# Optimization experiments

Hardware: AMD Instinct MI355X
Metric: run time of the kernel (lower is better)

## Reference

```python
import jax, jax.numpy as jnp
import numpy as np

N_E = 16384
E_DIM = 64
GROUPS = 4
N_E_GROUP = N_E // GROUPS  # 4096
B, H, W = 16, 32, 32


def _l2norm(x):
    # matches F.normalize(p=2, dim=-1) with eps=1e-12
    n = jnp.linalg.norm(x, axis=-1, keepdims=True)
    return x / jnp.maximum(n, 1e-12)


def setup_inputs() -> dict:
    key = jax.random.key(0)
    k1, k2 = jax.random.split(key)
    z_groups = jax.random.normal(k1, (B, GROUPS * E_DIM, H, W), dtype=jnp.float32)
    emb = jax.random.uniform(k2, (N_E, E_DIM), minval=-1.0 / N_E, maxval=1.0 / N_E,
                             dtype=jnp.float32)
    emb = _l2norm(emb)  # module normalizes codebook at init when l2_norm=True
    return {"z_groups": z_groups, "embedding": emb}


def reference(z_groups, embedding):
    # Eval-mode forward (no EMA/random-restart buffer updates, losses are 0).
    b, c, h, w = z_groups.shape
    # split channels into groups: b (g*c) h w -> b h w g c
    z = z_groups.reshape(b, GROUPS, E_DIM, h, w).transpose(0, 3, 4, 1, 2)
    z = _l2norm(z)                                     # l2_norm=True path
    zf = z.reshape(-1, GROUPS, E_DIM)                  # [N, g, c]
    emb = _l2norm(embedding.reshape(GROUPS, N_E_GROUP, E_DIM))  # [g, k, c]

    # d = -|z|^2 - |e|^2 + 2 z.e  (negative squared distance), argmax = nearest
    d = (2.0 * jnp.einsum('ngc,gkc->ngk', zf, emb)
         - jnp.sum(zf * zf, axis=-1)[..., None]
         - jnp.sum(emb * emb, axis=-1)[None, :, :])    # [N, g, k]
    idx = jnp.argmax(d, axis=-1)                       # [N, g]

    zq = emb[jnp.arange(GROUPS)[None, :], idx]         # [N, g, c] gather
    zq = zf + jax.lax.stop_gradient(zq - zf)           # straight-through

    # b h w g c -> b (g*c) h w
    quant = zq.reshape(b, h, w, GROUPS, E_DIM).transpose(0, 3, 4, 1, 2)
    quant = quant.reshape(b, GROUPS * E_DIM, h, w)

    vq_loss = jnp.zeros((GROUPS,), jnp.float32)
    commit_loss = jnp.zeros((GROUPS,), jnp.float32)
    codebook_usage = jnp.zeros((GROUPS,), jnp.float32)

    # perplexity / min_encodings correspond to the last group (loop semantics)
    min_encodings = jax.nn.one_hot(idx[:, -1], N_E_GROUP, dtype=quant.dtype)
    avg_probs = jnp.mean(min_encodings, axis=0)
    perplexity = jnp.exp(-jnp.sum(avg_probs * jnp.log(avg_probs + 1e-10)))

    return (quant, vq_loss, commit_loss, codebook_usage,
            perplexity, min_encodings, idx)
```

## Files before the change

### kernel.cpp

```cpp
#include <hip/hip_runtime.h>
#include <hip/hip_bf16.h>
#include <math.h>

#define N_E      16384
#define E_DIM    64
#define GROUPS   4
#define N_E_G    4096
#define NQ       16384

#define OFF_QUANT   0L
#define OFF_VQLOSS  4194304L
#define OFF_PERP    4194316L
#define OFF_MINENC  4194317L
#define OFF_IDX     71303181L

#define WS_EN     0L
#define WS_EN2    1048576L
#define WS_ENHI   1064960L
#define WS_ZNR    1589248L
#define WS_ZHI    5783552L
#define WS_HIST   7880704L
#define WS_IDX3   7884800L

typedef float  float4v  __attribute__((ext_vector_type(4)));
typedef short  short8   __attribute__((ext_vector_type(8)));

static __device__ __forceinline__ ushort f2bf(float x) {
    __hip_bfloat16 h = __float2bfloat16(x);
    union { __hip_bfloat16 h; ushort u; } cv; cv.h = h;
    return cv.u;
}

__global__ void norm_emb_kernel(const float* __restrict__ emb,
                                float* __restrict__ en, float* __restrict__ en2,
                                ushort* __restrict__ ehi) {
    int gid  = blockIdx.x * blockDim.x + threadIdx.x;
    int code = gid >> 6;
    int lane = threadIdx.x & 63;
    if (code >= N_E) return;
    float x = emb[code * 64 + lane];
    float ss = x * x;
    #pragma unroll
    for (int off = 32; off; off >>= 1) ss += __shfl_xor(ss, off, 64);
    float v = x / fmaxf(sqrtf(ss), 1e-12f);
    en[code * 64 + lane]  = v;
    ehi[code * 64 + lane] = f2bf(v);
    float s2 = v * v;
    #pragma unroll
    for (int off = 32; off; off >>= 1) s2 += __shfl_xor(s2, off, 64);
    if (lane == 0) en2[code] = s2;
}

__global__ void norm_z_kernel(const float* __restrict__ z,
                              float* __restrict__ znr, ushort* __restrict__ zhi) {
    __shared__ float rden[256];
    const int g  = blockIdx.y;
    const int n0 = blockIdx.x * 256;
    const int t  = threadIdx.x;

    {
        int n = n0 + t, b = n >> 10, hw = n & 1023;
        const float* src = z + (size_t)b * 262144 + (size_t)g * 65536 + hw;
        float ss = 0.f;
        for (int d = 0; d < 64; ++d) {
            float x = src[(size_t)d * 1024];
            ss = fmaf(x, x, ss);
        }
        rden[t] = fmaxf(sqrtf(ss), 1e-12f);
    }
    __syncthreads();

    for (int i = t; i < 256 * 16; i += 256) {
        int ql = i >> 4, d4 = (i & 15) * 4;
        int n = n0 + ql, b = n >> 10, hw = n & 1023;
        const float* src = z + (size_t)b * 262144 + (size_t)g * 65536 + hw;
        float den = rden[ql];
        float v0 = src[(size_t)(d4 + 0) * 1024] / den;
        float v1 = src[(size_t)(d4 + 1) * 1024] / den;
        float v2 = src[(size_t)(d4 + 2) * 1024] / den;
        float v3 = src[(size_t)(d4 + 3) * 1024] / den;
        float4v f = {v0, v1, v2, v3};
        *(float4v*)(znr + ((size_t)g * NQ + n) * 64 + d4) = f;
        ushort u0 = f2bf(v0), u1 = f2bf(v1), u2 = f2bf(v2), u3 = f2bf(v3);
        ushort4 u = {u0, u1, u2, u3};
        *(ushort4*)(zhi + ((size_t)g * NQ + n) * 64 + d4) = u;
    }
}

#define CAP  64
#define TAU  0.017f
__global__ __launch_bounds__(256, 2)
void vq_cand_kernel(const ushort* __restrict__ zhi, const ushort* __restrict__ ehi,
                    const float* __restrict__ znr, const float* __restrict__ en,
                    const float* __restrict__ en2,
                    float* __restrict__ out, int* __restrict__ idx3,
                    int* __restrict__ hist) {
    __shared__ ushort eA[128 * 64];
    __shared__ int    cnt[128];
    __shared__ int    cand[128 * CAP];
    __shared__ int    bks[128];

    const int g  = blockIdx.y;
    const int q0 = blockIdx.x * 128;
    const int t  = threadIdx.x;
    const int wave = t >> 6, lane = t & 63;
    const int l15 = lane & 15, quad = lane >> 4;
    const int qhalf = wave & 1, chalf = wave >> 1;

    if (t < 128) cnt[t] = 0;

    short8 bfrag[4][2];
    {
        const ushort* zq = zhi + ((size_t)g * NQ + q0 + qhalf * 64 + l15) * 64 + quad * 8;
        #pragma unroll
        for (int u = 0; u < 4; ++u)
            #pragma unroll
            for (int ks = 0; ks < 2; ++ks)
                bfrag[u][ks] = *(const short8*)(zq + (size_t)u * 16 * 64 + ks * 32);
    }

    float Mrun[4];
    #pragma unroll
    for (int u = 0; u < 4; ++u) Mrun[u] = -3.4e38f;

    for (int tile = 0; tile < 32; ++tile) {
        const int j0 = tile * 128;
        __syncthreads();
        {
            int c = t >> 1, half = t & 1;
            const ushort* src = ehi + ((size_t)g * N_E_G + j0 + c) * 64 + half * 32;
            #pragma unroll
            for (int qq = 0; qq < 4; ++qq) {
                int chunk = half * 4 + qq;
                short8 v = *(const short8*)(src + qq * 8);
                *(short8*)&eA[c * 64 + ((chunk ^ (c & 7)) * 8)] = v;
            }
        }
        __syncthreads();

        short8 afrag[4][2];
        #pragma unroll
        for (int cs = 0; cs < 4; ++cs) {
            int c = chalf * 64 + cs * 16 + l15;
            #pragma unroll
            for (int ks = 0; ks < 2; ++ks) {
                int chunk = ks * 4 + quad;
                afrag[cs][ks] = *(const short8*)&eA[c * 64 + ((chunk ^ (c & 7)) * 8)];
            }
        }

        float4v acc[4][4];
        #pragma unroll
        for (int cs = 0; cs < 4; ++cs)
            #pragma unroll
            for (int u = 0; u < 4; ++u) {
                float4v zz = {0.f, 0.f, 0.f, 0.f};
                acc[cs][u] = __builtin_amdgcn_mfma_f32_16x16x32_bf16(
                                 afrag[cs][0], bfrag[u][0], zz, 0, 0, 0);
                acc[cs][u] = __builtin_amdgcn_mfma_f32_16x16x32_bf16(
                                 afrag[cs][1], bfrag[u][1], acc[cs][u], 0, 0, 0);
            }

        #pragma unroll
        for (int u = 0; u < 4; ++u) {
            float m = acc[0][u][0];
            #pragma unroll
            for (int cs = 0; cs < 4; ++cs)
                #pragma unroll
                for (int r = 0; r < 4; ++r) m = fmaxf(m, acc[cs][u][r]);
            float m2 = fmaxf(m, __shfl_xor(m, 16, 64));
            float m4 = fmaxf(m2, __shfl_xor(m2, 32, 64));
            Mrun[u] = fmaxf(Mrun[u], m4);
            float thr = Mrun[u] - TAU;
            if (m >= thr) {
                int ql = qhalf * 64 + u * 16 + l15;
                #pragma unroll
                for (int cs = 0; cs < 4; ++cs)
                    #pragma unroll
                    for (int r = 0; r < 4; ++r)
                        if (acc[cs][u][r] >= thr) {
                            int cidx = j0 + chalf * 64 + cs * 16 + quad * 4 + r;
                            int slot = atomicAdd(&cnt[ql], 1);
                            if (slot < CAP) cand[ql * CAP + slot] = cidx;
                        }
            }
        }
    }
    __syncthreads();

    if (t < 128) {
        int q = q0 + t;
        float za[64];
        const float4v* zp = (const float4v*)(znr + ((size_t)g * NQ + q) * 64);
        #pragma unroll
        for (int i = 0; i < 16; ++i) {
            float4v v = zp[i];
            za[i*4+0] = v[0]; za[i*4+1] = v[1]; za[i*4+2] = v[2]; za[i*4+3] = v[3];
        }
        int nc = cnt[t]; if (nc > CAP) nc = CAP;
        float best = -3.4e38f; int bk = 0x7fffffff;
        for (int s = 0; s < nc; ++s) {
            int c = cand[t * CAP + s];
            const float* ev = en + ((size_t)g * N_E_G + c) * 64;
            float a = 0.f;
            #pragma unroll
            for (int k = 0; k < 64; ++k) a = fmaf(za[k], ev[k], a);
            float d = 2.f * a - en2[g * N_E_G + c];
            if (d > best || (d == best && c < bk)) { best = d; bk = c; }
        }
        if (bk == 0x7fffffff) bk = 0;
        bks[t] = bk;
        out[OFF_IDX + (size_t)q * 4 + g] = (float)bk;
        if (g == 3) { idx3[q] = bk; atomicAdd(&hist[bk], 1); }
    }
    __syncthreads();

    for (int i = t; i < 128 * 64; i += 256) {
        int d = i >> 7, m = i & 127;
        int n = q0 + m, b = n >> 10, hw = n & 1023;
        out[OFF_QUANT + (size_t)b * 262144 + (size_t)(g * 64 + d) * 1024 + hw] =
            en[((size_t)g * N_E_G + bks[m]) * 64 + d];
    }
}

__global__ void fill_zero_kernel(float* __restrict__ out) {
    const long n  = OFF_IDX - OFF_VQLOSS;
    const long n4 = n >> 2;
    float4v* p4 = (float4v*)(out + OFF_VQLOSS);
    long i = (long)blockIdx.x * blockDim.x + threadIdx.x;
    long stride = (long)gridDim.x * blockDim.x;
    float4v z = {0.f, 0.f, 0.f, 0.f};
    for (long j = i; j < n4; j += stride) p4[j] = z;
    if (i == 0) {
        float* p = out + OFF_VQLOSS;
        for (long j = n4 * 4; j < n; ++j) p[j] = 0.f;
    }
}

__global__ void scatter_ones_kernel(const int* __restrict__ idx3,
                                    float* __restrict__ out) {
    int r = blockIdx.x * blockDim.x + threadIdx.x;
    if (r < NQ) out[OFF_MINENC + (size_t)r * N_E_G + idx3[r]] = 1.0f;
}

__global__ void perplexity_kernel(const int* __restrict__ hist,
                                  float* __restrict__ out) {
    __shared__ float s[256];
    int t = threadIdx.x;
    float acc = 0.f;
    for (int k = t; k < N_E_G; k += 256) {
        float p = (float)hist[k] * (1.0f / 16384.0f);
        acc += p * logf(p + 1e-10f);
    }
    s[t] = acc;
    __syncthreads();
    for (int o = 128; o; o >>= 1) {
        if (t < o) s[t] += s[t + o];
        __syncthreads();
    }
    if (t == 0) out[OFF_PERP] = expf(-s[0]);
}

extern "C" void kernel_launch(void* const* d_in, const int* in_sizes, int n_in,
                              void* d_out, int out_size, void* d_ws, size_t ws_size,
                              hipStream_t stream) {
    const float* z_groups = (const float*)d_in[0];
    const float* emb      = (const float*)d_in[1];
    float* out = (float*)d_out;
    float* ws  = (float*)d_ws;

    float*  en   = ws + WS_EN;
    float*  en2  = ws + WS_EN2;
    ushort* ehi  = (ushort*)(ws + WS_ENHI);
    float*  znr  = ws + WS_ZNR;
    ushort* zhi  = (ushort*)(ws + WS_ZHI);
    int*    hist = (int*)(ws + WS_HIST);
    int*    idx3 = (int*)(ws + WS_IDX3);

    fill_zero_kernel<<<4096, 256, 0, stream>>>(out);
    norm_emb_kernel<<<N_E / 4, 256, 0, stream>>>(emb, en, en2, ehi);
    norm_z_kernel<<<dim3(NQ / 256, GROUPS), 256, 0, stream>>>(z_groups, znr, zhi);
    hipMemsetAsync(hist, 0, N_E_G * sizeof(int), stream);

    vq_cand_kernel<<<dim3(NQ / 128, GROUPS), 256, 0, stream>>>(
        zhi, ehi, znr, en, en2, out, idx3, hist);

    scatter_ones_kernel<<<NQ / 256, 256, 0, stream>>>(idx3, out);
    perplexity_kernel<<<1, 256, 0, stream>>>(hist, out);
}
```

Before: 481.0 us.

## Load codebook fragments from global with register double-buffering, fuse scatter, use memset

The candidate kernel stops staging codebook tiles through LDS with two barriers per tile. Each wave now loads its bf16 MFMA fragments straight from global memory, prefetching the next tile into a second register set. The one-hot scatter is folded into the candidate kernel, the zero-fill kernel becomes hipMemsetAsync, and z normalization goes through a padded LDS transpose so reads and writes are coalesced. The costs are higher register pressure and more global/L2 traffic for codebook reads, since waves no longer share a staged tile.

```diff
diff --git a/kernel.cpp b/kernel.cpp
--- a/kernel.cpp
+++ b/kernel.cpp
@@ -20,14 +20,12 @@
 #define WS_ZNR    1589248L
 #define WS_ZHI    5783552L
 #define WS_HIST   7880704L
-#define WS_IDX3   7884800L
 
 typedef float  float4v  __attribute__((ext_vector_type(4)));
 typedef short  short8   __attribute__((ext_vector_type(8)));
 
 static __device__ __forceinline__ ushort f2bf(float x) {
-    __hip_bfloat16 h = __float2bfloat16(x);
-    union { __hip_bfloat16 h; ushort u; } cv; cv.h = h;
+    union { __hip_bfloat16 h; ushort u; } cv; cv.h = __float2bfloat16(x);
     return cv.u;
 }
 
@@ -53,37 +51,37 @@
 
 __global__ void norm_z_kernel(const float* __restrict__ z,
                               float* __restrict__ znr, ushort* __restrict__ zhi) {
-    __shared__ float rden[256];
+    __shared__ float tile[64 * 65];
+    __shared__ float rden[64];
+
     const int g  = blockIdx.y;
-    const int n0 = blockIdx.x * 256;
+    const int n0 = blockIdx.x * 64;
     const int t  = threadIdx.x;
-
-    {
-        int n = n0 + t, b = n >> 10, hw = n & 1023;
-        const float* src = z + (size_t)b * 262144 + (size_t)g * 65536 + hw;
+    const int b  = n0 >> 10, hw0 = n0 & 1023;
+    const float* src = z + (size_t)b * 262144 + (size_t)g * 65536 + hw0;
+
+    for (int i = t; i < 4096; i += 256) {
+        int d = i >> 6, nl = i & 63;
+        tile[d * 65 + nl] = src[(size_t)d * 1024 + nl];
+    }
+    __syncthreads();
+
+    if (t < 64) {
         float ss = 0.f;
         for (int d = 0; d < 64; ++d) {
-            float x = src[(size_t)d * 1024];
+            float x = tile[d * 65 + t];
             ss = fmaf(x, x, ss);
         }
         rden[t] = fmaxf(sqrtf(ss), 1e-12f);
     }
     __syncthreads();
 
-    for (int i = t; i < 256 * 16; i += 256) {
-        int ql = i >> 4, d4 = (i & 15) * 4;
-        int n = n0 + ql, b = n >> 10, hw = n & 1023;
-        const float* src = z + (size_t)b * 262144 + (size_t)g * 65536 + hw;
-        float den = rden[ql];
-        float v0 = src[(size_t)(d4 + 0) * 1024] / den;
-        float v1 = src[(size_t)(d4 + 1) * 1024] / den;
-        float v2 = src[(size_t)(d4 + 2) * 1024] / den;
-        float v3 = src[(size_t)(d4 + 3) * 1024] / den;
-        float4v f = {v0, v1, v2, v3};
-        *(float4v*)(znr + ((size_t)g * NQ + n) * 64 + d4) = f;
-        ushort u0 = f2bf(v0), u1 = f2bf(v1), u2 = f2bf(v2), u3 = f2bf(v3);
-        ushort4 u = {u0, u1, u2, u3};
-        *(ushort4*)(zhi + ((size_t)g * NQ + n) * 64 + d4) = u;
+    for (int i = t; i < 4096; i += 256) {
+        int q = i >> 6, d = i & 63;
+        float v = tile[d * 65 + q] / rden[q];
+        size_t o = ((size_t)g * NQ + n0 + q) * 64 + d;
+        znr[o] = v;
+        zhi[o] = f2bf(v);
     }
 }
 
@@ -92,13 +90,11 @@
 __global__ __launch_bounds__(256, 2)
 void vq_cand_kernel(const ushort* __restrict__ zhi, const ushort* __restrict__ ehi,
                     const float* __restrict__ znr, const float* __restrict__ en,
-                    const float* __restrict__ en2,
-                    float* __restrict__ out, int* __restrict__ idx3,
+                    const float* __restrict__ en2, float* __restrict__ out,
                     int* __restrict__ hist) {
-    __shared__ ushort eA[128 * 64];
-    __shared__ int    cnt[128];
-    __shared__ int    cand[128 * CAP];
-    __shared__ int    bks[128];
+    __shared__ int cnt[128];
+    __shared__ int cand[128 * CAP];
+    __shared__ int bks[128];
 
     const int g  = blockIdx.y;
     const int q0 = blockIdx.x * 128;
@@ -116,51 +112,45 @@
         for (int u = 0; u < 4; ++u)
             #pragma unroll
             for (int ks = 0; ks < 2; ++ks)
-                bfrag[u][ks] = *(const short8*)(zq + (size_t)u * 16 * 64 + ks * 32);
-    }
+                bfrag[u][ks] = *(const short8*)(zq + u * 16 * 64 + ks * 32);
+    }
+    __syncthreads();
+
+    const ushort* abase = ehi + (size_t)g * N_E_G * 64
+                        + (size_t)(chalf * 64 + l15) * 64 + quad * 8;
 
     float Mrun[4];
     #pragma unroll
     for (int u = 0; u < 4; ++u) Mrun[u] = -3.4e38f;
 
-    for (int tile = 0; tile < 32; ++tile) {
-        const int j0 = tile * 128;
-        __syncthreads();
-        {
-            int c = t >> 1, half = t & 1;
-            const ushort* src = ehi + ((size_t)g * N_E_G + j0 + c) * 64 + half * 32;
-            #pragma unroll
-            for (int qq = 0; qq < 4; ++qq) {
-                int chunk = half * 4 + qq;
-                short8 v = *(const short8*)(src + qq * 8);
-                *(short8*)&eA[c * 64 + ((chunk ^ (c & 7)) * 8)] = v;
-            }
-        }
-        __syncthreads();
-
-        short8 afrag[4][2];
-        #pragma unroll
-        for (int cs = 0; cs < 4; ++cs) {
-            int c = chalf * 64 + cs * 16 + l15;
-            #pragma unroll
-            for (int ks = 0; ks < 2; ++ks) {
-                int chunk = ks * 4 + quad;
-                afrag[cs][ks] = *(const short8*)&eA[c * 64 + ((chunk ^ (c & 7)) * 8)];
-            }
-        }
-
+    short8 afA[4][2], afB[4][2];
+    #pragma unroll
+    for (int cs = 0; cs < 4; ++cs)
+        #pragma unroll
+        for (int ks = 0; ks < 2; ++ks)
+            afA[cs][ks] = *(const short8*)(abase + (size_t)(cs * 16) * 64 + ks * 32);
+
+    auto do_tile = [&](short8 (&A)[4][2], short8 (&P)[4][2], int tile) {
+        if (tile + 1 < 32) {
+            const ushort* p = abase + (size_t)((tile + 1) * 128) * 64;
+            #pragma unroll
+            for (int cs = 0; cs < 4; ++cs)
+                #pragma unroll
+                for (int ks = 0; ks < 2; ++ks)
+                    P[cs][ks] = *(const short8*)(p + (size_t)(cs * 16) * 64 + ks * 32);
+        }
         float4v acc[4][4];
         #pragma unroll
         for (int cs = 0; cs < 4; ++cs)
             #pragma unroll
             for (int u = 0; u < 4; ++u) {
                 float4v zz = {0.f, 0.f, 0.f, 0.f};
+                float4v tmp = __builtin_amdgcn_mfma_f32_16x16x32_bf16(
+                                  A[cs][0], bfrag[u][0], zz, 0, 0, 0);
                 acc[cs][u] = __builtin_amdgcn_mfma_f32_16x16x32_bf16(
-                                 afrag[cs][0], bfrag[u][0], zz, 0, 0, 0);
-                acc[cs][u] = __builtin_amdgcn_mfma_f32_16x16x32_bf16(
-                                 afrag[cs][1], bfrag[u][1], acc[cs][u], 0, 0, 0);
+                                  A[cs][1], bfrag[u][1], tmp, 0, 0, 0);
             }
-
+        const int j0 = tile * 128;
         #pragma unroll
         for (int u = 0; u < 4; ++u) {
             float m = acc[0][u][0];
@@ -185,6 +175,11 @@
                         }
             }
         }
+    };
+
+    for (int tt = 0; tt < 32; tt += 2) {
+        do_tile(afA, afB, tt);
+        do_tile(afB, afA, tt + 1);
     }
     __syncthreads();
 
@@ -211,7 +206,10 @@
         if (bk == 0x7fffffff) bk = 0;
         bks[t] = bk;
         out[OFF_IDX + (size_t)q * 4 + g] = (float)bk;
-        if (g == 3) { idx3[q] = bk; atomicAdd(&hist[bk], 1); }
+        if (g == 3) {
+            atomicAdd(&hist[bk], 1);
+            out[OFF_MINENC + (size_t)q * N_E_G + bk] = 1.0f;
+        }
     }
     __syncthreads();
 
@@ -221,26 +219,6 @@
         out[OFF_QUANT + (size_t)b * 262144 + (size_t)(g * 64 + d) * 1024 + hw] =
             en[((size_t)g * N_E_G + bks[m]) * 64 + d];
     }
-}
-
-__global__ void fill_zero_kernel(float* __restrict__ out) {
-    const long n  = OFF_IDX - OFF_VQLOSS;
-    const long n4 = n >> 2;
-    float4v* p4 = (float4v*)(out + OFF_VQLOSS);
-    long i = (long)blockIdx.x * blockDim.x + threadIdx.x;
-    long stride = (long)gridDim.x * blockDim.x;
-    float4v z = {0.f, 0.f, 0.f, 0.f};
-    for (long j = i; j < n4; j += stride) p4[j] = z;
-    if (i == 0) {
-        float* p = out + OFF_VQLOSS;
-        for (long j = n4 * 4; j < n; ++j) p[j] = 0.f;
-    }
-}
-
-__global__ void scatter_ones_kernel(const int* __restrict__ idx3,
-                                    float* __restrict__ out) {
-    int r = blockIdx.x * blockDim.x + threadIdx.x;
-    if (r < NQ) out[OFF_MINENC + (size_t)r * N_E_G + idx3[r]] = 1.0f;
 }
 
 __global__ void perplexity_kernel(const int* __restrict__ hist,
@@ -275,16 +253,15 @@
     float*  znr  = ws + WS_ZNR;
     ushort* zhi  = (ushort*)(ws + WS_ZHI);
     int*    hist = (int*)(ws + WS_HIST);
-    int*    idx3 = (int*)(ws + WS_IDX3);
-
-    fill_zero_kernel<<<4096, 256, 0, stream>>>(out);
+
+    hipMemsetAsync(out + OFF_VQLOSS, 0, (OFF_IDX - OFF_VQLOSS) * sizeof(float), stream);
+    hipMemsetAsync(hist, 0, N_E_G * sizeof(int), stream);
+
     norm_emb_kernel<<<N_E / 4, 256, 0, stream>>>(emb, en, en2, ehi);
-    norm_z_kernel<<<dim3(NQ / 256, GROUPS), 256, 0, stream>>>(z_groups, znr, zhi);
-    hipMemsetAsync(hist, 0, N_E_G * sizeof(int), stream);
+    norm_z_kernel<<<dim3(NQ / 64, GROUPS), 256, 0, stream>>>(z_groups, znr, zhi);
 
     vq_cand_kernel<<<dim3(NQ / 128, GROUPS), 256, 0, stream>>>(
-        zhi, ehi, znr, en, en2, out, idx3, hist);
-
-    scatter_ones_kernel<<<NQ / 256, 256, 0, stream>>>(idx3, out);
+        zhi, ehi, znr, en, en2, out, hist);
+
     perplexity_kernel<<<1, 256, 0, stream>>>(hist, out);
 }
```

Result: faster. 432.7 us (-10.0%).
